# Kernel tuning notes

Hardware: AMD Instinct MI355X
Metric: run time of the kernel (lower is better)

## Reference

```python
import jax, jax.numpy as jnp
import numpy as np

# basis X = [1s, 2s, 1p, 2p, 1d] -> angular momenta
LI = [0, 0, 1, 1, 2]
NORBS = [2 * l + 1 for l in LI]          # [1,1,3,3,5]
NORB = int(sum(NORBS))                    # 13 = full_basis_norb


def _build_maps():
    """Precompute static gather maps replacing the nested python loops.

    P[r, c]  : index into the edge feature vector (all orbital pairs, row-major)
    Nm[r, c] : index into the node feature vector (i<=j pairs; i>j reads the
               transposed element of block (j, i), matching the torch code).
    """
    offs = np.concatenate([[0], np.cumsum(NORBS)])
    n = len(NORBS)
    pair_start = np.zeros((n, n), dtype=np.int64)
    c = 0
    for i in range(n):
        for j in range(n):
            pair_start[i, j] = c
            c += NORBS[i] * NORBS[j]
    node_start = {}
    c = 0
    for i in range(n):
        for j in range(i, n):
            node_start[(i, j)] = c
            c += NORBS[i] * NORBS[j]
    orb_of = np.concatenate([[i] * NORBS[i] for i in range(n)])
    P = np.zeros((NORB, NORB), dtype=np.int64)
    Nm = np.zeros((NORB, NORB), dtype=np.int64)
    for r in range(NORB):
        i = int(orb_of[r]); ri = r - offs[i]
        for cc in range(NORB):
            j = int(orb_of[cc]); cj = cc - offs[j]
            P[r, cc] = pair_start[i, j] + ri * NORBS[j] + cj
            if i <= j:
                Nm[r, cc] = node_start[(i, j)] + ri * NORBS[j] + cj
            else:
                Nm[r, cc] = node_start[(j, i)] + cj * NORBS[i] + ri
    return jnp.asarray(P), jnp.asarray(Nm)


def setup_inputs() -> dict:
    key = jax.random.key(0)
    k1, k2, k3, k4, k5 = jax.random.split(key, 5)
    N, E, K = 200, 4800, 8
    edge_features = jax.random.normal(k1, (E, NORB * NORB), dtype=jnp.float32)
    node_features = jax.random.normal(k2, (N, 107), dtype=jnp.float32)
    kpoints = jax.random.uniform(k3, (K, 3), dtype=jnp.float32)
    edge_cell_shift = jax.random.normal(k4, (E, 3), dtype=jnp.float32)
    edge_index = jax.random.randint(k5, (2, E), 0, N, dtype=jnp.int64)
    atom_types = jnp.zeros((N,), dtype=jnp.int64)
    return {"edge_features": edge_features, "node_features": node_features,
            "kpoints": kpoints, "edge_cell_shift": edge_cell_shift,
            "edge_index": edge_index, "atom_types": atom_types}


def reference(edge_features, node_features, kpoints, edge_cell_shift,
              edge_index, atom_types):
    P, Nm = _build_maps()
    E = edge_features.shape[0]
    N = node_features.shape[0]
    K = kpoints.shape[0]

    # orbital-pair block assembly (replaces nested python loops): gathers
    hop = edge_features[:, P]        # [E, 13, 13]
    onsite = node_features[:, Nm]    # [N, 13, 13] (symmetric layout built into Nm)

    # phase factors exp(-i 2 pi k . R)   [K, E]
    phases = jnp.exp(-2j * jnp.pi * (kpoints @ edge_cell_shift.T)).astype(jnp.complex64)

    # H(k) as [K, N, 13, N, 13]
    H = jnp.zeros((K, N, NORB, N, NORB), dtype=jnp.complex64)
    idx = jnp.arange(N)
    # onsite: 0.5 * block on the diagonal (symmetrized later)
    diag = (0.5 * onsite).astype(jnp.complex64)[:, None]           # [N,1,13,13]
    H = H.at[:, idx, :, idx, :].set(jnp.broadcast_to(diag, (N, K, NORB, NORB)))
    # hopping: scatter-add hblock * phase into block (src, dst)
    src, dst = edge_index[0], edge_index[1]
    contrib = phases[:, :, None, None] * hop[None].astype(jnp.complex64)  # [K,E,13,13]
    H = H.at[:, src, :, dst, :].add(jnp.transpose(contrib, (1, 0, 2, 3)))

    H = H.reshape(K, N * NORB, N * NORB)
    H = H + jnp.conj(jnp.swapaxes(H, 1, 2))
    return H
```

## Files before the change

kernel.cpp:

```cpp
#include <hip/hip_runtime.h>


__device__ __forceinline__ void orb_of(int r, int& i, int& ri, int& nv) {
    if (r < 1)      { i = 0; ri = r;     nv = 1; }
    else if (r < 2) { i = 1; ri = r - 1; nv = 1; }
    else if (r < 5) { i = 2; ri = r - 2; nv = 3; }
    else if (r < 8) { i = 3; ri = r - 5; nv = 3; }
    else            { i = 4; ri = r - 8; nv = 5; }
}
__device__ __forceinline__ int offs_of(int i) {
    return i == 0 ? 0 : (i == 1 ? 1 : (i == 2 ? 2 : (i == 3 ? 5 : 8)));
}
__device__ __forceinline__ int rowstart_of(int i) {
    return i == 0 ? 0 : (i == 1 ? 13 : (i == 2 ? 25 : (i == 3 ? 58 : 82)));
}
__device__ __forceinline__ int pmap(int r, int c) {
    int i, ri, nvi, j, cj, nvj;
    orb_of(r, i, ri, nvi);
    orb_of(c, j, cj, nvj);
    return 13 * offs_of(i) + nvi * offs_of(j) + ri * nvj + cj;
}
__device__ __forceinline__ int nmap(int r, int c) {
    int i, ri, nvi, j, cj, nvj;
    orb_of(r, i, ri, nvi);
    orb_of(c, j, cj, nvj);
    if (i <= j)
        return rowstart_of(i) + nvi * (offs_of(j) - offs_of(i)) + ri * nvj + cj;
    else
        return rowstart_of(j) + nvj * (offs_of(i) - offs_of(j)) + cj * nvi + ri;
}

constexpr float TWO_PI = 6.28318530717958647692f;
constexpr int CAPC = 128;

__global__ __launch_bounds__(256) void bucket_fill(const int* __restrict__ eidx,
                                                   int* __restrict__ cnt,
                                                   int* __restrict__ bkt,
                                                   int E) {
    int e = blockIdx.x * 256 + threadIdx.x;
    if (e >= E) return;
    int s = eidx[e], d = eidx[E + e];
    int p = atomicAdd(&cnt[s], 1);
    if (p < CAPC) bkt[s * CAPC + p] = (d << 18) | (e << 1);
    int q = atomicAdd(&cnt[d], 1);
    if (q < CAPC) bkt[d * CAPC + q] = (s << 18) | (e << 1) | 1;
}

template <int CPLX, int KB>
__global__ __launch_bounds__(256) void hr2hk_main(const float* __restrict__ ef,
                                                  const float* __restrict__ nf,
                                                  const float* __restrict__ kp,
                                                  const float* __restrict__ ecs,
                                                  const int*   __restrict__ eidx,
                                                  const int*   __restrict__ cnt,
                                                  const int*   __restrict__ bkt,
                                                  float* __restrict__ out,
                                                  int N, int E, int K) {
    const int DIM  = N * 13;
    const int rowf = CPLX ? DIM * 2 : DIM;
    const int row4 = rowf >> 2;
    const int a   = blockIdx.x % DIM;
    const int kg  = blockIdx.x / DIM;
    const int n1  = a / 13, r = a - n1 * 13;
    const int k0  = kg * KB;
    const int kb  = (K - k0 < KB) ? (K - k0) : KB;
    const int tid = threadIdx.x;

    __shared__ float h_sh[CAPC * 13];
    __shared__ float ph_sh[CAPC * KB * (CPLX ? 2 : 1)];
    __shared__ int   lst[CAPC];
    __shared__ int   head[256];
    __shared__ int   nxt[CAPC];
    __shared__ float dseg[13];
    __shared__ int   pm_s[13], pm_d[13];
    __shared__ float kp_sh[KB * 3];

    const int cnt_n = cnt[n1];
    const int cb = (cnt_n > CAPC) ? 0 : cnt_n;

    head[tid & 255] = -1;
    if (tid < 13) {
        pm_s[tid] = pmap(r, tid);
        pm_d[tid] = pmap(tid, r);
        dseg[tid] = 0.5f * (nf[n1 * 107 + nmap(r, tid)] + nf[n1 * 107 + nmap(tid, r)]);
    }
    if (tid < kb * 3) kp_sh[tid] = kp[k0 * 3 + tid];
    if (tid < cb) lst[tid] = bkt[n1 * CAPC + tid];
    __syncthreads();

    if (tid < cb) {
        int o = (int)((unsigned)lst[tid] >> 18);
        nxt[tid] = atomicExch(&head[o], tid);
    }
    for (int t = tid; t < cb * KB; t += 256) {
        int li = t / KB, kk = t - li * KB;
        if (kk < kb) {
            int entry = lst[li];
            int e = (int)(((unsigned)entry >> 1) & 0x1FFFF);
            float sx = ecs[e * 3], sy = ecs[e * 3 + 1], sz = ecs[e * 3 + 2];
            float dot = kp_sh[kk * 3]     * sx
                      + kp_sh[kk * 3 + 1] * sy
                      + kp_sh[kk * 3 + 2] * sz;
            float th = TWO_PI * dot;
            if (CPLX) {
                float sn, co;
                sincosf(th, &sn, &co);
                ph_sh[(li * KB + kk) * 2]     = co;
                ph_sh[(li * KB + kk) * 2 + 1] = (entry & 1) ? sn : -sn;
            } else {
                ph_sh[li * KB + kk] = cosf(th);
            }
        }
    }
    for (int t = tid; t < cb * 13; t += 256) {
        int li = t / 13, c = t - li * 13;
        int entry = lst[li];
        int e = (int)(((unsigned)entry >> 1) & 0x1FFFF);
        h_sh[li * 13 + c] = ef[(long)e * 169 + ((entry & 1) ? pm_d[c] : pm_s[c])];
    }
    __syncthreads();

    for (int t = tid; t < row4; t += 256) {
        float acc[KB][4];
        if (CPLX) {
#pragma unroll
            for (int j = 0; j < 2; ++j) {
                int col = 2 * t + j;
                int o = (int)((unsigned)col / 13u);
                int cc = col - o * 13;
                float dre = (o == n1) ? dseg[cc] : 0.f;
#pragma unroll
                for (int kk = 0; kk < KB; ++kk) {
                    acc[kk][2 * j]     = dre;
                    acc[kk][2 * j + 1] = 0.f;
                }
                for (int li = head[o]; li >= 0; li = nxt[li]) {
                    float h = h_sh[li * 13 + cc];
#pragma unroll
                    for (int kk = 0; kk < KB; ++kk) {
                        acc[kk][2 * j]     += h * ph_sh[(li * KB + kk) * 2];
                        acc[kk][2 * j + 1] += h * ph_sh[(li * KB + kk) * 2 + 1];
                    }
                }
            }
        } else {
#pragma unroll
            for (int j = 0; j < 4; ++j) {
                int col = 4 * t + j;
                int o = (int)((unsigned)col / 13u);
                int cc = col - o * 13;
                float d = (o == n1) ? dseg[cc] : 0.f;
#pragma unroll
                for (int kk = 0; kk < KB; ++kk) acc[kk][j] = d;
                for (int li = head[o]; li >= 0; li = nxt[li]) {
                    float h = h_sh[li * 13 + cc];
#pragma unroll
                    for (int kk = 0; kk < KB; ++kk)
                        acc[kk][j] += h * ph_sh[li * KB + kk];
                }
            }
        }
#pragma unroll
        for (int kk = 0; kk < KB; ++kk) {
            if (kk < kb) {
                long base = ((long)(k0 + kk) * DIM + a) * (long)rowf;
                float4 v = {acc[kk][0], acc[kk][1], acc[kk][2], acc[kk][3]};
                ((float4*)(out + base))[t] = v;
            }
        }
    }

    if (cnt_n > CAPC) {
        __syncthreads();
        for (int t = tid; t < 2 * E; t += 256) {
            int e = t >> 1, side = t & 1;
            int node  = side ? eidx[E + e] : eidx[e];
            if (node != n1) continue;
            int other = side ? eidx[e] : eidx[E + e];
            float sx = ecs[e * 3], sy = ecs[e * 3 + 1], sz = ecs[e * 3 + 2];
            for (int kk = 0; kk < kb; ++kk) {
                float dot = kp_sh[kk * 3] * sx + kp_sh[kk * 3 + 1] * sy
                          + kp_sh[kk * 3 + 2] * sz;
                float th = TWO_PI * dot;
                long base = ((long)(k0 + kk) * DIM + a) * (long)rowf;
                if (CPLX) {
                    float sn, co;
                    sincosf(th, &sn, &co);
                    for (int c = 0; c < 13; ++c) {
                        float h = ef[(long)e * 169 + (side ? pm_d[c] : pm_s[c])];
                        atomicAdd(out + base + (other * 13 + c) * 2,     h * co);
                        atomicAdd(out + base + (other * 13 + c) * 2 + 1, side ? h * sn : -h * sn);
                    }
                } else {
                    float co = cosf(th);
                    for (int c = 0; c < 13; ++c) {
                        float h = ef[(long)e * 169 + (side ? pm_d[c] : pm_s[c])];
                        atomicAdd(out + base + other * 13 + c, h * co);
                    }
                }
            }
        }
    }
}


__global__ __launch_bounds__(256) void zero_kernel(float* __restrict__ out, long n) {
    long n4 = n >> 2;
    float4* out4 = (float4*)out;
    long i = (long)blockIdx.x * blockDim.x + threadIdx.x;
    long stride = (long)gridDim.x * blockDim.x;
    const float4 z = {0.f, 0.f, 0.f, 0.f};
    for (long t = i; t < n4; t += stride) out4[t] = z;
    if (i == 0) for (long j = n4 << 2; j < n; ++j) out[j] = 0.f;
}

template <int CPLX>
__global__ __launch_bounds__(256) void diag_kernel(const float* __restrict__ nf,
                                                   float* __restrict__ out,
                                                   int N, int total, long out_lim) {
    int t = blockIdx.x * blockDim.x + threadIdx.x;
    if (t >= total) return;
    int per_k = N * 169;
    int k = t / per_k, rem = t - k * per_k;
    int n = rem / 169, idx = rem - n * 169;
    int r = idx / 13, c = idx - r * 13;
    float v = 0.5f * (nf[n * 107 + nmap(r, c)] + nf[n * 107 + nmap(c, r)]);
    long DIM = (long)N * 13;
    long off = ((long)k * DIM + (long)n * 13 + r) * DIM + (long)n * 13 + c;
    if (CPLX) off *= 2;
    if (off >= 0 && off < out_lim) out[off] = v;
}

template <int CPLX>
__global__ __launch_bounds__(256) void edge_kernel(const float* __restrict__ ef,
                                                   const float* __restrict__ kp,
                                                   const float* __restrict__ ecs,
                                                   const int*   __restrict__ eidx,
                                                   float* __restrict__ out,
                                                   int N, int E, int K, long out_lim) {
    const int e = blockIdx.x;
    __shared__ float hop_sh[169];
    __shared__ float cos_sh[32];
    __shared__ float sin_sh[32];
    const int tid = threadIdx.x;
    const int r = tid / 13, c = tid - r * 13;

    if (tid < 169) hop_sh[tid] = ef[(long)e * 169 + pmap(r, c)];
    if (tid < K && tid < 32) {
        float sx = ecs[e * 3 + 0], sy = ecs[e * 3 + 1], sz = ecs[e * 3 + 2];
        float dot = kp[tid * 3 + 0] * sx + kp[tid * 3 + 1] * sy + kp[tid * 3 + 2] * sz;
        float th = TWO_PI * dot;
        float s, co;
        sincosf(th, &s, &co);
        cos_sh[tid] = co;
        sin_sh[tid] = s;
    }
    __syncthreads();
    if (tid >= 169) return;

    const int src = eidx[e];
    const int dst = eidx[E + e];
    const long DIM = (long)N * 13;
    const long SL  = DIM * DIM;
    const float h  = hop_sh[tid];
    const float ht = hop_sh[c * 13 + r];
    const long base1 = ((long)src * 13 + r) * DIM + (long)dst * 13 + c;
    const long base2 = ((long)dst * 13 + r) * DIM + (long)src * 13 + c;

    for (int k = 0; k < K; ++k) {
        float co = cos_sh[k & 31];
        float si = sin_sh[k & 31];
        if (CPLX) {
            long o1 = ((long)k * SL + base1) * 2;
            long o2 = ((long)k * SL + base2) * 2;
            if (o1 >= 0 && o1 + 1 < out_lim) {
                atomicAdd(out + o1,      h * co);
                atomicAdd(out + o1 + 1, -h * si);
            }
            if (o2 >= 0 && o2 + 1 < out_lim) {
                atomicAdd(out + o2,     ht * co);
                atomicAdd(out + o2 + 1, ht * si);
            }
        } else {
            long o1 = (long)k * SL + base1;
            long o2 = (long)k * SL + base2;
            if (o1 >= 0 && o1 < out_lim) atomicAdd(out + o1, h * co);
            if (o2 >= 0 && o2 < out_lim) atomicAdd(out + o2, ht * co);
        }
    }
}


extern "C" void kernel_launch(void* const* d_in, const int* in_sizes, int n_in,
                              void* d_out, int out_size, void* d_ws, size_t ws_size,
                              hipStream_t stream) {
    const float* ef   = (const float*)d_in[0];
    const float* nf   = (const float*)d_in[1];
    const float* kp   = (const float*)d_in[2];
    const float* ecs  = (const float*)d_in[3];
    const int*   eidx = (const int*)d_in[4];

    const int E = in_sizes[0] / 169;
    const int N = in_sizes[1] / 107;
    const int K = in_sizes[2] / 3;

    float* out = (float*)d_out;
    const long DIM  = (long)N * 13;
    const long SL   = DIM * DIM;
    const long full = (long)K * SL * 2;
    const int  cplx = ((long)out_size >= full) ? 1 : 0;
    const long out_lim = (long)out_size;

    const int  rowf = (int)DIM * (cplx ? 2 : 1);
    const long ws_ints = (long)N + (long)N * CAPC;
    const bool fast_ok = (N >= 1) && (N <= 256) && (K >= 1) &&
                         (E >= 1) && (E < 131072) && (rowf % 4 == 0) &&
                         (ws_size >= (size_t)(ws_ints * 4)) &&
                         ((long)out_size == (long)K * SL * (cplx ? 2 : 1));

    if (fast_ok) {
        int* cnt = (int*)d_ws;
        int* bkt = cnt + N;

        hipMemsetAsync(cnt, 0, (size_t)N * sizeof(int), stream);
        bucket_fill<<<(E + 255) / 256, 256, 0, stream>>>(eidx, cnt, bkt, E);

        if (cplx) {
            constexpr int KB = 4;
            int kgroups = (K + KB - 1) / KB;
            hr2hk_main<1, KB><<<kgroups * (int)DIM, 256, 0, stream>>>(
                ef, nf, kp, ecs, eidx, cnt, bkt, out, N, E, K);
        } else {
            constexpr int KB = 8;
            int kgroups = (K + KB - 1) / KB;
            hr2hk_main<0, KB><<<kgroups * (int)DIM, 256, 0, stream>>>(
                ef, nf, kp, ecs, eidx, cnt, bkt, out, N, E, K);
        }
    } else {
        zero_kernel<<<2048, 256, 0, stream>>>(out, out_lim);
        int total_diag = K * N * 169;
        int blocks_diag = (total_diag + 255) / 256;
        if (cplx) {
            diag_kernel<1><<<blocks_diag, 256, 0, stream>>>(nf, out, N, total_diag, out_lim);
            edge_kernel<1><<<E, 256, 0, stream>>>(ef, kp, ecs, eidx, out, N, E, K, out_lim);
        } else {
            diag_kernel<0><<<blocks_diag, 256, 0, stream>>>(nf, out, N, total_diag, out_lim);
            edge_kernel<0><<<E, 256, 0, stream>>>(ef, kp, ecs, eidx, out, N, E, K, out_lim);
        }
    }
}
```

Measured before the change: 54.27 us.

## Process two output rows per block to share bucket and phase setup

Each block now handles two orbital rows of the same node instead of one, so the bucket list, linked-list build and phase sincos computation are amortized over two rows. The grid shrinks to 7 blocks per node per k-group. The phase array is transposed to k-major layout and the bucket capacity is reduced to cut shared memory. The trade-offs are fewer blocks, longer per-block serial work, and a higher chance of nodes overflowing the smaller capacity into the slow atomic fallback.

```diff
diff --git a/kernel.cpp b/kernel.cpp
--- a/kernel.cpp
+++ b/kernel.cpp
@@ -31,7 +31,7 @@
 }
 
 constexpr float TWO_PI = 6.28318530717958647692f;
-constexpr int CAPC = 128;
+constexpr int CAPC = 96;
 
 __global__ __launch_bounds__(256) void bucket_fill(const int* __restrict__ eidx,
                                                    int* __restrict__ cnt,
@@ -59,30 +59,38 @@
     const int DIM  = N * 13;
     const int rowf = CPLX ? DIM * 2 : DIM;
     const int row4 = rowf >> 2;
-    const int a   = blockIdx.x % DIM;
-    const int kg  = blockIdx.x / DIM;
-    const int n1  = a / 13, r = a - n1 * 13;
+    const int b   = blockIdx.x;
+    const int rp  = b % 7;
+    const int n1  = (b / 7) % N;
+    const int kg  = b / (7 * N);
+    const int r0  = 2 * rp;
+    const int nr  = (rp == 6) ? 1 : 2;
     const int k0  = kg * KB;
     const int kb  = (K - k0 < KB) ? (K - k0) : KB;
     const int tid = threadIdx.x;
 
-    __shared__ float h_sh[CAPC * 13];
+    __shared__ float h_sh[2][CAPC * 13];
     __shared__ float ph_sh[CAPC * KB * (CPLX ? 2 : 1)];
     __shared__ int   lst[CAPC];
     __shared__ int   head[256];
     __shared__ int   nxt[CAPC];
-    __shared__ float dseg[13];
-    __shared__ int   pm_s[13], pm_d[13];
+    __shared__ float dseg[2][13];
+    __shared__ int   pm_s[2][13], pm_d[2][13];
     __shared__ float kp_sh[KB * 3];
 
     const int cnt_n = cnt[n1];
     const int cb = (cnt_n > CAPC) ? 0 : cnt_n;
 
-    head[tid & 255] = -1;
-    if (tid < 13) {
-        pm_s[tid] = pmap(r, tid);
-        pm_d[tid] = pmap(tid, r);
-        dseg[tid] = 0.5f * (nf[n1 * 107 + nmap(r, tid)] + nf[n1 * 107 + nmap(tid, r)]);
+    head[tid] = -1;
+    if (tid < 26) {
+        int ir = tid / 13, cc = tid - ir * 13;
+        if (ir < nr) {
+            int rr = r0 + ir;
+            pm_s[ir][cc] = pmap(rr, cc);
+            pm_d[ir][cc] = pmap(cc, rr);
+            dseg[ir][cc] = 0.5f * (nf[n1 * 107 + nmap(rr, cc)]
+                                 + nf[n1 * 107 + nmap(cc, rr)]);
+        }
     }
     if (tid < kb * 3) kp_sh[tid] = kp[k0 * 3 + tid];
     if (tid < cb) lst[tid] = bkt[n1 * CAPC + tid];
@@ -105,97 +113,107 @@
             if (CPLX) {
                 float sn, co;
                 sincosf(th, &sn, &co);
-                ph_sh[(li * KB + kk) * 2]     = co;
-                ph_sh[(li * KB + kk) * 2 + 1] = (entry & 1) ? sn : -sn;
+                ph_sh[(kk * CAPC + li) * 2]     = co;
+                ph_sh[(kk * CAPC + li) * 2 + 1] = (entry & 1) ? sn : -sn;
             } else {
-                ph_sh[li * KB + kk] = cosf(th);
-            }
-        }
-    }
-    for (int t = tid; t < cb * 13; t += 256) {
-        int li = t / 13, c = t - li * 13;
+                ph_sh[kk * CAPC + li] = cosf(th);
+            }
+        }
+    }
+    for (int t = tid; t < nr * cb * 13; t += 256) {
+        int ir = t / (cb * 13);
+        int rem = t - ir * cb * 13;
+        int li = rem / 13, c = rem - li * 13;
         int entry = lst[li];
         int e = (int)(((unsigned)entry >> 1) & 0x1FFFF);
-        h_sh[li * 13 + c] = ef[(long)e * 169 + ((entry & 1) ? pm_d[c] : pm_s[c])];
+        h_sh[ir][li * 13 + c] =
+            ef[(long)e * 169 + ((entry & 1) ? pm_d[ir][c] : pm_s[ir][c])];
     }
     __syncthreads();
 
-    for (int t = tid; t < row4; t += 256) {
-        float acc[KB][4];
-        if (CPLX) {
-#pragma unroll
-            for (int j = 0; j < 2; ++j) {
-                int col = 2 * t + j;
-                int o = (int)((unsigned)col / 13u);
-                int cc = col - o * 13;
-                float dre = (o == n1) ? dseg[cc] : 0.f;
-#pragma unroll
-                for (int kk = 0; kk < KB; ++kk) {
-                    acc[kk][2 * j]     = dre;
-                    acc[kk][2 * j + 1] = 0.f;
-                }
-                for (int li = head[o]; li >= 0; li = nxt[li]) {
-                    float h = h_sh[li * 13 + cc];
+    for (int ir = 0; ir < nr; ++ir) {
+        const int a = n1 * 13 + r0 + ir;
+        for (int t = tid; t < row4; t += 256) {
+            float acc[KB][4];
+            if (CPLX) {
+#pragma unroll
+                for (int j = 0; j < 2; ++j) {
+                    int col = 2 * t + j;
+                    int o = (int)((unsigned)col / 13u);
+                    int cc = col - o * 13;
+                    float dre = (o == n1) ? dseg[ir][cc] : 0.f;
 #pragma unroll
                     for (int kk = 0; kk < KB; ++kk) {
-                        acc[kk][2 * j]     += h * ph_sh[(li * KB + kk) * 2];
-                        acc[kk][2 * j + 1] += h * ph_sh[(li * KB + kk) * 2 + 1];
+                        acc[kk][2 * j]     = dre;
+                        acc[kk][2 * j + 1] = 0.f;
+                    }
+                    for (int li = head[o]; li >= 0; li = nxt[li]) {
+                        float h = h_sh[ir][li * 13 + cc];
+#pragma unroll
+                        for (int kk = 0; kk < KB; ++kk) {
+                            acc[kk][2 * j]     += h * ph_sh[(kk * CAPC + li) * 2];
+                            acc[kk][2 * j + 1] += h * ph_sh[(kk * CAPC + li) * 2 + 1];
+                        }
                     }
                 }
-            }
-        } else {
-#pragma unroll
-            for (int j = 0; j < 4; ++j) {
-                int col = 4 * t + j;
-                int o = (int)((unsigned)col / 13u);
-                int cc = col - o * 13;
-                float d = (o == n1) ? dseg[cc] : 0.f;
-#pragma unroll
-                for (int kk = 0; kk < KB; ++kk) acc[kk][j] = d;
-                for (int li = head[o]; li >= 0; li = nxt[li]) {
-                    float h = h_sh[li * 13 + cc];
-#pragma unroll
-                    for (int kk = 0; kk < KB; ++kk)
-                        acc[kk][j] += h * ph_sh[li * KB + kk];
+            } else {
+#pragma unroll
+                for (int j = 0; j < 4; ++j) {
+                    int col = 4 * t + j;
+                    int o = (int)((unsigned)col / 13u);
+                    int cc = col - o * 13;
+                    float d = (o == n1) ? dseg[ir][cc] : 0.f;
+#pragma unroll
+                    for (int kk = 0; kk < KB; ++kk) acc[kk][j] = d;
+                    for (int li = head[o]; li >= 0; li = nxt[li]) {
+                        float h = h_sh[ir][li * 13 + cc];
+#pragma unroll
+                        for (int kk = 0; kk < KB; ++kk)
+                            acc[kk][j] += h * ph_sh[kk * CAPC + li];
+                    }
                 }
             }
-        }
-#pragma unroll
-        for (int kk = 0; kk < KB; ++kk) {
-            if (kk < kb) {
-                long base = ((long)(k0 + kk) * DIM + a) * (long)rowf;
-                float4 v = {acc[kk][0], acc[kk][1], acc[kk][2], acc[kk][3]};
-                ((float4*)(out + base))[t] = v;
+#pragma unroll
+            for (int kk = 0; kk < KB; ++kk) {
+                if (kk < kb) {
+                    long base = ((long)(k0 + kk) * DIM + a) * (long)rowf;
+                    float4 v = {acc[kk][0], acc[kk][1], acc[kk][2], acc[kk][3]};
+                    ((float4*)(out + base))[t] = v;
+                }
             }
         }
     }
 
     if (cnt_n > CAPC) {
         __syncthreads();
-        for (int t = tid; t < 2 * E; t += 256) {
-            int e = t >> 1, side = t & 1;
-            int node  = side ? eidx[E + e] : eidx[e];
-            if (node != n1) continue;
-            int other = side ? eidx[e] : eidx[E + e];
-            float sx = ecs[e * 3], sy = ecs[e * 3 + 1], sz = ecs[e * 3 + 2];
-            for (int kk = 0; kk < kb; ++kk) {
-                float dot = kp_sh[kk * 3] * sx + kp_sh[kk * 3 + 1] * sy
-                          + kp_sh[kk * 3 + 2] * sz;
-                float th = TWO_PI * dot;
-                long base = ((long)(k0 + kk) * DIM + a) * (long)rowf;
-                if (CPLX) {
-                    float sn, co;
-                    sincosf(th, &sn, &co);
-                    for (int c = 0; c < 13; ++c) {
-                        float h = ef[(long)e * 169 + (side ? pm_d[c] : pm_s[c])];
-                        atomicAdd(out + base + (other * 13 + c) * 2,     h * co);
-                        atomicAdd(out + base + (other * 13 + c) * 2 + 1, side ? h * sn : -h * sn);
-                    }
-                } else {
-                    float co = cosf(th);
-                    for (int c = 0; c < 13; ++c) {
-                        float h = ef[(long)e * 169 + (side ? pm_d[c] : pm_s[c])];
-                        atomicAdd(out + base + other * 13 + c, h * co);
+        for (int ir = 0; ir < nr; ++ir) {
+            const int a = n1 * 13 + r0 + ir;
+            for (int t = tid; t < 2 * E; t += 256) {
+                int e = t >> 1, side = t & 1;
+                int node  = side ? eidx[E + e] : eidx[e];
+                if (node != n1) continue;
+                int other = side ? eidx[e] : eidx[E + e];
+                float sx = ecs[e * 3], sy = ecs[e * 3 + 1], sz = ecs[e * 3 + 2];
+                for (int kk = 0; kk < kb; ++kk) {
+                    float dot = kp_sh[kk * 3] * sx + kp_sh[kk * 3 + 1] * sy
+                              + kp_sh[kk * 3 + 2] * sz;
+                    float th = TWO_PI * dot;
+                    long base = ((long)(k0 + kk) * DIM + a) * (long)rowf;
+                    if (CPLX) {
+                        float sn, co;
+                        sincosf(th, &sn, &co);
+                        for (int c = 0; c < 13; ++c) {
+                            float h = ef[(long)e * 169 + (side ? pm_d[ir][c] : pm_s[ir][c])];
+                            atomicAdd(out + base + (other * 13 + c) * 2,     h * co);
+                            atomicAdd(out + base + (other * 13 + c) * 2 + 1,
+                                      side ? h * sn : -h * sn);
+                        }
+                    } else {
+                        float co = cosf(th);
+                        for (int c = 0; c < 13; ++c) {
+                            float h = ef[(long)e * 169 + (side ? pm_d[ir][c] : pm_s[ir][c])];
+                            atomicAdd(out + base + other * 13 + c, h * co);
+                        }
                     }
                 }
             }
@@ -328,12 +346,12 @@
         if (cplx) {
             constexpr int KB = 4;
             int kgroups = (K + KB - 1) / KB;
-            hr2hk_main<1, KB><<<kgroups * (int)DIM, 256, 0, stream>>>(
+            hr2hk_main<1, KB><<<kgroups * N * 7, 256, 0, stream>>>(
                 ef, nf, kp, ecs, eidx, cnt, bkt, out, N, E, K);
         } else {
             constexpr int KB = 8;
             int kgroups = (K + KB - 1) / KB;
-            hr2hk_main<0, KB><<<kgroups * (int)DIM, 256, 0, stream>>>(
+            hr2hk_main<0, KB><<<kgroups * N * 7, 256, 0, stream>>>(
                 ef, nf, kp, ecs, eidx, cnt, bkt, out, N, E, K);
         }
     } else {
```

Result: slower. 56.97 us (+5.0%).

## Precompute per-edge phases and permuted hopping blocks in a pre-pass kernel

Applied to the files above, without the earlier changes.

Replaces the bucket-fill kernel with a per-edge pre-pass. The pre-pass computes the K phase factors once per edge and writes the hopping block in both row-permuted and transposed layouts to workspace, alongside the bucketing. The main kernel then reads contiguous precomputed rows and phases instead of recomputing sincos for every (row, k-group) block and doing scattered gathers through pmap. This costs an extra E-block launch, extra workspace traffic (2×169 floats per edge) and a K<=64 limit on the fast path.

```diff
diff --git a/kernel.cpp b/kernel.cpp
--- a/kernel.cpp
+++ b/kernel.cpp
@@ -33,21 +33,50 @@
 constexpr float TWO_PI = 6.28318530717958647692f;
 constexpr int CAPC = 128;
 
-__global__ __launch_bounds__(256) void bucket_fill(const int* __restrict__ eidx,
-                                                   int* __restrict__ cnt,
-                                                   int* __restrict__ bkt,
-                                                   int E) {
-    int e = blockIdx.x * 256 + threadIdx.x;
-    if (e >= E) return;
-    int s = eidx[e], d = eidx[E + e];
-    int p = atomicAdd(&cnt[s], 1);
-    if (p < CAPC) bkt[s * CAPC + p] = (d << 18) | (e << 1);
-    int q = atomicAdd(&cnt[d], 1);
-    if (q < CAPC) bkt[d * CAPC + q] = (s << 18) | (e << 1) | 1;
+template <int CPLX>
+__global__ __launch_bounds__(256) void edge_pre(const float* __restrict__ ef,
+                                                const float* __restrict__ kp,
+                                                const float* __restrict__ ecs,
+                                                const int*   __restrict__ eidx,
+                                                float* __restrict__ phases,
+                                                float* __restrict__ hop_pre,
+                                                float* __restrict__ hopT_pre,
+                                                int* __restrict__ cnt,
+                                                int* __restrict__ bkt,
+                                                int E, int K) {
+    const int e = blockIdx.x;
+    const int tid = threadIdx.x;
+    if (tid < 169) {
+        int r = tid / 13, c = tid - r * 13;
+        hop_pre [(long)e * 169 + tid] = ef[(long)e * 169 + pmap(r, c)];
+        hopT_pre[(long)e * 169 + tid] = ef[(long)e * 169 + pmap(c, r)];
+    }
+    if (tid < K) {
+        float sx = ecs[e * 3], sy = ecs[e * 3 + 1], sz = ecs[e * 3 + 2];
+        float dot = kp[tid * 3] * sx + kp[tid * 3 + 1] * sy + kp[tid * 3 + 2] * sz;
+        float th = TWO_PI * dot;
+        if (CPLX) {
+            float sn, co;
+            sincosf(th, &sn, &co);
+            phases[((long)e * K + tid) * 2]     = co;
+            phases[((long)e * K + tid) * 2 + 1] = sn;
+        } else {
+            phases[(long)e * K + tid] = cosf(th);
+        }
+    }
+    if (tid == 0) {
+        int s = eidx[e], d = eidx[E + e];
+        int p = atomicAdd(&cnt[s], 1);
+        if (p < CAPC) bkt[s * CAPC + p] = (d << 18) | (e << 1);
+        int q = atomicAdd(&cnt[d], 1);
+        if (q < CAPC) bkt[d * CAPC + q] = (s << 18) | (e << 1) | 1;
+    }
 }
 
 template <int CPLX, int KB>
-__global__ __launch_bounds__(256) void hr2hk_main(const float* __restrict__ ef,
+__global__ __launch_bounds__(256) void hr2hk_main(const float* __restrict__ hop_pre,
+                                                  const float* __restrict__ hopT_pre,
+                                                  const float* __restrict__ phases,
                                                   const float* __restrict__ nf,
                                                   const float* __restrict__ kp,
                                                   const float* __restrict__ ecs,
@@ -78,7 +107,7 @@
     const int cnt_n = cnt[n1];
     const int cb = (cnt_n > CAPC) ? 0 : cnt_n;
 
-    head[tid & 255] = -1;
+    head[tid] = -1;
     if (tid < 13) {
         pm_s[tid] = pmap(r, tid);
         pm_d[tid] = pmap(tid, r);
@@ -97,18 +126,13 @@
         if (kk < kb) {
             int entry = lst[li];
             int e = (int)(((unsigned)entry >> 1) & 0x1FFFF);
-            float sx = ecs[e * 3], sy = ecs[e * 3 + 1], sz = ecs[e * 3 + 2];
-            float dot = kp_sh[kk * 3]     * sx
-                      + kp_sh[kk * 3 + 1] * sy
-                      + kp_sh[kk * 3 + 2] * sz;
-            float th = TWO_PI * dot;
             if (CPLX) {
-                float sn, co;
-                sincosf(th, &sn, &co);
+                float co = phases[((long)e * K + k0 + kk) * 2];
+                float sn = phases[((long)e * K + k0 + kk) * 2 + 1];
                 ph_sh[(li * KB + kk) * 2]     = co;
                 ph_sh[(li * KB + kk) * 2 + 1] = (entry & 1) ? sn : -sn;
             } else {
-                ph_sh[li * KB + kk] = cosf(th);
+                ph_sh[li * KB + kk] = phases[(long)e * K + k0 + kk];
             }
         }
     }
@@ -116,7 +140,8 @@
         int li = t / 13, c = t - li * 13;
         int entry = lst[li];
         int e = (int)(((unsigned)entry >> 1) & 0x1FFFF);
-        h_sh[li * 13 + c] = ef[(long)e * 169 + ((entry & 1) ? pm_d[c] : pm_s[c])];
+        const float* hp = (entry & 1) ? hopT_pre : hop_pre;
+        h_sh[li * 13 + c] = hp[(long)e * 169 + r * 13 + c];
     }
     __syncthreads();
 
@@ -187,14 +212,14 @@
                     float sn, co;
                     sincosf(th, &sn, &co);
                     for (int c = 0; c < 13; ++c) {
-                        float h = ef[(long)e * 169 + (side ? pm_d[c] : pm_s[c])];
+                        float h = (side ? hopT_pre : hop_pre)[(long)e * 169 + r * 13 + c];
                         atomicAdd(out + base + (other * 13 + c) * 2,     h * co);
                         atomicAdd(out + base + (other * 13 + c) * 2 + 1, side ? h * sn : -h * sn);
                     }
                 } else {
                     float co = cosf(th);
                     for (int c = 0; c < 13; ++c) {
-                        float h = ef[(long)e * 169 + (side ? pm_d[c] : pm_s[c])];
+                        float h = (side ? hopT_pre : hop_pre)[(long)e * 169 + r * 13 + c];
                         atomicAdd(out + base + other * 13 + c, h * co);
                     }
                 }
@@ -312,29 +337,40 @@
     const long out_lim = (long)out_size;
 
     const int  rowf = (int)DIM * (cplx ? 2 : 1);
-    const long ws_ints = (long)N + (long)N * CAPC;
-    const bool fast_ok = (N >= 1) && (N <= 256) && (K >= 1) &&
+    const long o_ph   = 0;
+    const long o_hop  = o_ph + (long)E * K * 2;
+    const long o_hopT = o_hop + (long)E * 169;
+    const long f_tot  = o_hopT + (long)E * 169;
+    const long i_base = (f_tot + 3) & ~3L;
+    const long ws_req = (i_base + (long)N + (long)N * CAPC) * 4;
+    const bool fast_ok = (N >= 1) && (N <= 256) && (K >= 1) && (K <= 64) &&
                          (E >= 1) && (E < 131072) && (rowf % 4 == 0) &&
-                         (ws_size >= (size_t)(ws_ints * 4)) &&
+                         (ws_size >= (size_t)ws_req) &&
                          ((long)out_size == (long)K * SL * (cplx ? 2 : 1));
 
     if (fast_ok) {
-        int* cnt = (int*)d_ws;
+        float* wf = (float*)d_ws;
+        float* phases   = wf + o_ph;
+        float* hop_pre  = wf + o_hop;
+        float* hopT_pre = wf + o_hopT;
+        int* cnt = (int*)d_ws + i_base;
         int* bkt = cnt + N;
 
         hipMemsetAsync(cnt, 0, (size_t)N * sizeof(int), stream);
-        bucket_fill<<<(E + 255) / 256, 256, 0, stream>>>(eidx, cnt, bkt, E);
-
         if (cplx) {
+            edge_pre<1><<<E, 256, 0, stream>>>(ef, kp, ecs, eidx, phases,
+                                               hop_pre, hopT_pre, cnt, bkt, E, K);
             constexpr int KB = 4;
             int kgroups = (K + KB - 1) / KB;
             hr2hk_main<1, KB><<<kgroups * (int)DIM, 256, 0, stream>>>(
-                ef, nf, kp, ecs, eidx, cnt, bkt, out, N, E, K);
-        } else {
+                hop_pre, hopT_pre, phases, nf, kp, ecs, eidx, cnt, bkt, out, N, E, K);
+        } else {
+            edge_pre<0><<<E, 256, 0, stream>>>(ef, kp, ecs, eidx, phases,
+                                               hop_pre, hopT_pre, cnt, bkt, E, K);
             constexpr int KB = 8;
             int kgroups = (K + KB - 1) / KB;
             hr2hk_main<0, KB><<<kgroups * (int)DIM, 256, 0, stream>>>(
-                ef, nf, kp, ecs, eidx, cnt, bkt, out, N, E, K);
+                hop_pre, hopT_pre, phases, nf, kp, ecs, eidx, cnt, bkt, out, N, E, K);
         }
     } else {
         zero_kernel<<<2048, 256, 0, stream>>>(out, out_lim);
```

Result: slower. 65.13 us (+20.0%).
